# Kernel tuning notes

Hardware: AMD Instinct MI355X
Metric: run time of the kernel (lower is better)

The kernel has to match this reference:

```python
import jax, jax.numpy as jnp
import numpy as np

N_NODES = 100000
N_EDGES = 3200000
F_IN = 512
HIDDEN = 16
N_CLASSES = 16


def setup_inputs() -> dict:
    key = jax.random.key(0)
    k1, k2, k3, k4 = jax.random.split(key, 4)
    x = jax.random.normal(k1, (N_NODES, F_IN), dtype=jnp.float32)
    edge_index = jax.random.randint(k2, (2, N_EDGES), 0, N_NODES, dtype=jnp.int32)
    # Glorot-style init for GCN weights
    W1 = jax.random.normal(k3, (F_IN, HIDDEN), dtype=jnp.float32) * np.float32(np.sqrt(2.0 / (F_IN + HIDDEN)))
    b1 = jnp.zeros((HIDDEN,), dtype=jnp.float32)
    W2 = jax.random.normal(k4, (HIDDEN, N_CLASSES), dtype=jnp.float32) * np.float32(np.sqrt(2.0 / (HIDDEN + N_CLASSES)))
    b2 = jnp.zeros((N_CLASSES,), dtype=jnp.float32)
    return {"x": x, "W1": W1, "b1": b1, "W2": W2, "b2": b2, "edge_index": edge_index}


def _gcn_conv(x, src, dst, W, b, n_nodes):
    """PyG GCNConv: h = x @ W, then symmetric-normalized aggregation with self-loops, + bias."""
    h = x @ W  # [N, out]
    # degrees include self-loops (edge weight 1.0 everywhere)
    ones = jnp.ones(src.shape[0], dtype=h.dtype)
    deg = jax.ops.segment_sum(ones, dst, num_segments=n_nodes) + 1.0  # +1 for self-loop
    dinv = jax.lax.rsqrt(deg)  # deg >= 1, no zero guard needed
    norm = dinv[src] * dinv[dst]  # [E]
    agg = jax.ops.segment_sum(h[src] * norm[:, None], dst, num_segments=n_nodes)
    # self-loop contribution: norm_ii = 1/deg_i
    agg = agg + h * (dinv * dinv)[:, None]
    return agg + b


def reference(x, W1, b1, W2, b2, edge_index):
    src, dst = edge_index[0], edge_index[1]
    n = x.shape[0]
    h = jax.nn.relu(_gcn_conv(x, src, dst, W1, b1, n))
    # dropout is identity in eval mode
    out = _gcn_conv(h, src, dst, W2, b2, n)
    return jax.nn.log_softmax(out, axis=1)
```

## Files before the change

kernel.cpp:

```cpp
#include <hip/hip_runtime.h>
#include <math.h>

constexpr int N_NODES = 100000;
constexpr int N_EDGES = 3200000;
constexpr int F_IN    = 512;
constexpr int HID     = 16;

constexpr int NPAD = 100352;

constexpr int B_BITS = 8;
constexpr int NPB    = 1 << B_BITS;
constexpr int NBKT   = (N_NODES + NPB - 1) / NPB;
constexpr int SBLK   = 400;
constexpr int CHUNK  = N_EDGES / SBLK;
constexpr int CAP    = 10240;

typedef float f32x4 __attribute__((ext_vector_type(4)));
typedef short bfrag8 __attribute__((ext_vector_type(8)));

__device__ __forceinline__ unsigned short f2bf_rne(float f) {
    unsigned int u = __float_as_uint(f);
    u += 0x7FFFu + ((u >> 16) & 1u);
    return (unsigned short)(u >> 16);
}
__device__ __forceinline__ float bf2f(unsigned short u) {
    return __uint_as_float((unsigned int)u << 16);
}

__global__ __launch_bounds__(256) void prep_kernel(const float* __restrict__ W1,
                                                   unsigned short* __restrict__ w1t,
                                                   int* __restrict__ gcur,
                                                   unsigned short* __restrict__ hh_bf,
                                                   unsigned short* __restrict__ hh2_bf) {
    int i = blockIdx.x * 256 + threadIdx.x;
    if (i < F_IN * HID) {
        int k = i >> 4, n = i & 15;
        w1t[n * F_IN + k] = f2bf_rne(W1[i]);
    }
    if (i < NBKT) gcur[i] = i * CAP;
    if (i < 16) {
        hh_bf [N_NODES * 16 + i] = 0;
        hh2_bf[N_NODES * 16 + i] = 0;
    }
}

__global__ __launch_bounds__(1024) void bin_scatter_kernel(const int* __restrict__ src,
                                                           const int* __restrict__ dst,
                                                           int* __restrict__ gcur,
                                                           unsigned int* __restrict__ binned) {
    __shared__ int sdst[CHUNK];
    __shared__ int ssrc[CHUNK];
    __shared__ int cnt[NBKT];
    __shared__ int cur[NBKT];
    const int tid = threadIdx.x;
    for (int t = tid; t < NBKT; t += 1024) cnt[t] = 0;
    const int base = blockIdx.x * CHUNK;
    for (int i = tid; i < CHUNK; i += 1024) {
        sdst[i] = dst[base + i];
        ssrc[i] = src[base + i];
    }
    __syncthreads();
    for (int i = tid; i < CHUNK; i += 1024)
        atomicAdd(&cnt[sdst[i] >> B_BITS], 1);
    __syncthreads();
    for (int t = tid; t < NBKT; t += 1024)
        cur[t] = cnt[t] ? atomicAdd(&gcur[t], cnt[t]) : 0;
    __syncthreads();
    for (int i = tid; i < CHUNK; i += 1024) {
        int d = sdst[i];
        int b = d >> B_BITS;
        int pos = atomicAdd(&cur[b], 1);
        binned[pos] = ((unsigned)(d & (NPB - 1)) << 24) | (unsigned)ssrc[i];
    }
}

__global__ __launch_bounds__(1024) void csr_bucket_kernel(const unsigned int* __restrict__ binned,
                                                          const int* __restrict__ gcur,
                                                          int* __restrict__ row,
                                                          int* __restrict__ rowe,
                                                          int* __restrict__ csr,
                                                          float* __restrict__ dinv) {
    __shared__ unsigned int eb[CAP];
    __shared__ int deg[NPB];
    __shared__ int pre[NPB];
    __shared__ int cur[NPB];
    const int tid = threadIdx.x;
    const int b = blockIdx.x;
    const int e0 = b * CAP;
    int ne = gcur[b] - e0;
    if (ne > CAP) ne = CAP;
    if (ne < 0) ne = 0;

    if (tid < NPB) deg[tid] = 0;
    for (int i = tid; i < ne; i += 1024) eb[i] = binned[e0 + i];
    __syncthreads();
    for (int i = tid; i < ne; i += 1024)
        atomicAdd(&deg[eb[i] >> 24], 1);
    __syncthreads();
    if (tid < NPB) pre[tid] = (deg[tid] + 3) & ~3;
    __syncthreads();
    for (int off = 1; off < NPB; off <<= 1) {
        int v = 0;
        if (tid < NPB && tid >= off) v = pre[tid - off];
        __syncthreads();
        if (tid < NPB) pre[tid] += v;
        __syncthreads();
    }
    if (tid < NPB) {
        int excl = (tid == 0) ? 0 : pre[tid - 1];
        int start = e0 + excl;
        cur[tid] = start;
        int node = b * NPB + tid;
        if (node < N_NODES) {
            int pd = (deg[tid] + 3) & ~3;
            row[node]  = start;
            rowe[node] = start + pd;
            dinv[node] = rsqrtf((float)deg[tid] + 1.0f);
        }
    }
    __syncthreads();
    for (int i = tid; i < ne; i += 1024) {
        unsigned int v = eb[i];
        int pos = atomicAdd(&cur[v >> 24], 1);
        csr[pos] = (int)(v & 0xFFFFFFu);
    }
    if (tid < NPB) {
        int node = b * NPB + tid;
        if (node < N_NODES) {
            int d = deg[tid];
            int pd = (d + 3) & ~3;
            int s = e0 + ((tid == 0) ? 0 : pre[tid - 1]) + d;
            for (int q = d; q < pd; ++q) csr[s++] = N_NODES;
        }
    }
}

__global__ __launch_bounds__(256) void gemm1_kernel(const float* __restrict__ x,
                                                    const unsigned short* __restrict__ w1t,
                                                    const float* __restrict__ b1,
                                                    const float* __restrict__ dinv,
                                                    unsigned short* __restrict__ hh_bf,
                                                    float* __restrict__ aggs1) {
    const int tid  = threadIdx.x;
    const int lane = tid & 63;
    const int wv   = tid >> 6;
    const int m    = lane & 15;
    const int quad = lane >> 4;
    const int node0 = blockIdx.x * 64 + wv * 16;

    int gm = node0 + m; if (gm >= N_NODES) gm = N_NODES - 1;
    const float* arow = x + (size_t)gm * F_IN + quad * 8;

    bfrag8 bfr[16];
    const unsigned short* wbase = w1t + m * F_IN + quad * 8;
    #pragma unroll
    for (int t = 0; t < 16; ++t)
        bfr[t] = *(const bfrag8*)(wbase + t * 32);

    f32x4 acc = {0.f, 0.f, 0.f, 0.f};
    #pragma unroll 4
    for (int t = 0; t < 16; ++t) {
        float4 lo = *(const float4*)(arow + t * 32);
        float4 hi = *(const float4*)(arow + t * 32 + 4);
        bfrag8 afr;
        afr[0] = (short)f2bf_rne(lo.x); afr[1] = (short)f2bf_rne(lo.y);
        afr[2] = (short)f2bf_rne(lo.z); afr[3] = (short)f2bf_rne(lo.w);
        afr[4] = (short)f2bf_rne(hi.x); afr[5] = (short)f2bf_rne(hi.y);
        afr[6] = (short)f2bf_rne(hi.z); afr[7] = (short)f2bf_rne(hi.w);
        acc = __builtin_amdgcn_mfma_f32_16x16x32_bf16(afr, bfr[t], acc, 0, 0, 0);
    }

    const float b1j = b1[m];
    #pragma unroll
    for (int r = 0; r < 4; ++r) {
        int gn = node0 + quad * 4 + r;
        if (gn < N_NODES) {
            float dv = dinv[gn];
            float hv = acc[r] * dv;
            size_t o = (size_t)gn * 16 + m;
            hh_bf[o] = f2bf_rne(hv);
            aggs1[o] = hv * dv + b1j;
        }
    }
}

__global__ __launch_bounds__(256) void pull1_kernel(const unsigned short* __restrict__ hh_bf,
                                                    const float* __restrict__ aggs1,
                                                    const float* __restrict__ dinv,
                                                    const int* __restrict__ row,
                                                    const int* __restrict__ rowe,
                                                    const int* __restrict__ csr,
                                                    const float* __restrict__ W2,
                                                    const float* __restrict__ b2,
                                                    unsigned short* __restrict__ hh2_bf,
                                                    float* __restrict__ aggs2) {
    __shared__ f32x4 w2s[64];
    __shared__ f32x4 b2s[4];
    const int tid = threadIdx.x;
    if (tid < 64) w2s[tid] = ((const f32x4*)W2)[tid];
    if (tid < 4)  b2s[tid] = ((const f32x4*)b2)[tid];
    __syncthreads();

    int t = blockIdx.x * 256 + tid;
    int node = t >> 2;
    int l = t & 3;
    if (node >= N_NODES) return;

    int p = row[node], e = rowe[node];
    const unsigned short* hb = hh_bf + (l << 2);
    f32x4 a0 = {0,0,0,0}, a1 = {0,0,0,0}, a2 = {0,0,0,0}, a3 = {0,0,0,0};
    for (; p < e; p += 4) {
        int4 s = *(const int4*)(csr + p);
        ushort4 g0 = *(const ushort4*)(hb + (s.x << 4));
        ushort4 g1 = *(const ushort4*)(hb + (s.y << 4));
        ushort4 g2 = *(const ushort4*)(hb + (s.z << 4));
        ushort4 g3 = *(const ushort4*)(hb + (s.w << 4));
        a0.x += bf2f(g0.x); a0.y += bf2f(g0.y); a0.z += bf2f(g0.z); a0.w += bf2f(g0.w);
        a1.x += bf2f(g1.x); a1.y += bf2f(g1.y); a1.z += bf2f(g1.z); a1.w += bf2f(g1.w);
        a2.x += bf2f(g2.x); a2.y += bf2f(g2.y); a2.z += bf2f(g2.z); a2.w += bf2f(g2.w);
        a3.x += bf2f(g3.x); a3.y += bf2f(g3.y); a3.z += bf2f(g3.z); a3.w += bf2f(g3.w);
    }
    f32x4 a = (a0 + a1) + (a2 + a3);
    float dv = dinv[node];
    f32x4 base = *(const f32x4*)(aggs1 + ((size_t)node << 4) + (l << 2));
    float v[4];
    #pragma unroll
    for (int c = 0; c < 4; ++c) v[c] = fmaxf(base[c] + dv * a[c], 0.f);

    f32x4 h2 = {0.f, 0.f, 0.f, 0.f};
    #pragma unroll
    for (int k = 0; k < 16; ++k) {
        float vk = __shfl(v[k & 3], k >> 2, 4);
        f32x4 w = w2s[k * 4 + l];
        h2.x += vk * w.x; h2.y += vk * w.y; h2.z += vk * w.z; h2.w += vk * w.w;
    }
    f32x4 bb = b2s[l];
    ushort4 hs;
    f32x4 ag;
    float hv0 = h2.x * dv; hs.x = f2bf_rne(hv0); ag.x = hv0 * dv + bb.x;
    float hv1 = h2.y * dv; hs.y = f2bf_rne(hv1); ag.y = hv1 * dv + bb.y;
    float hv2 = h2.z * dv; hs.z = f2bf_rne(hv2); ag.z = hv2 * dv + bb.z;
    float hv3 = h2.w * dv; hs.w = f2bf_rne(hv3); ag.w = hv3 * dv + bb.w;
    size_t o = ((size_t)node << 4) + (l << 2);
    *(ushort4*)(hh2_bf + o) = hs;
    *(f32x4*)(aggs2 + o) = ag;
}

__global__ __launch_bounds__(256) void pull2_kernel(const unsigned short* __restrict__ hh2_bf,
                                                    const float* __restrict__ aggs2,
                                                    const float* __restrict__ dinv,
                                                    const int* __restrict__ row,
                                                    const int* __restrict__ rowe,
                                                    const int* __restrict__ csr,
                                                    float* __restrict__ out) {
    int t = blockIdx.x * 256 + threadIdx.x;
    int node = t >> 2;
    int l = t & 3;
    if (node >= N_NODES) return;

    int p = row[node], e = rowe[node];
    const unsigned short* hb = hh2_bf + (l << 2);
    f32x4 a0 = {0,0,0,0}, a1 = {0,0,0,0}, a2 = {0,0,0,0}, a3 = {0,0,0,0};
    for (; p < e; p += 4) {
        int4 s = *(const int4*)(csr + p);
        ushort4 g0 = *(const ushort4*)(hb + (s.x << 4));
        ushort4 g1 = *(const ushort4*)(hb + (s.y << 4));
        ushort4 g2 = *(const ushort4*)(hb + (s.z << 4));
        ushort4 g3 = *(const ushort4*)(hb + (s.w << 4));
        a0.x += bf2f(g0.x); a0.y += bf2f(g0.y); a0.z += bf2f(g0.z); a0.w += bf2f(g0.w);
        a1.x += bf2f(g1.x); a1.y += bf2f(g1.y); a1.z += bf2f(g1.z); a1.w += bf2f(g1.w);
        a2.x += bf2f(g2.x); a2.y += bf2f(g2.y); a2.z += bf2f(g2.z); a2.w += bf2f(g2.w);
        a3.x += bf2f(g3.x); a3.y += bf2f(g3.y); a3.z += bf2f(g3.z); a3.w += bf2f(g3.w);
    }
    f32x4 a = (a0 + a1) + (a2 + a3);
    float dv = dinv[node];
    f32x4 base = *(const f32x4*)(aggs2 + ((size_t)node << 4) + (l << 2));
    f32x4 o4;
    o4.x = base.x + dv * a.x; o4.y = base.y + dv * a.y;
    o4.z = base.z + dv * a.z; o4.w = base.w + dv * a.w;

    float m = fmaxf(fmaxf(o4.x, o4.y), fmaxf(o4.z, o4.w));
    m = fmaxf(m, __shfl_xor(m, 1));
    m = fmaxf(m, __shfl_xor(m, 2));
    float s = expf(o4.x - m) + expf(o4.y - m) + expf(o4.z - m) + expf(o4.w - m);
    s += __shfl_xor(s, 1);
    s += __shfl_xor(s, 2);
    float ls = m + logf(s);
    f32x4 r;
    r.x = o4.x - ls; r.y = o4.y - ls; r.z = o4.z - ls; r.w = o4.w - ls;
    *(f32x4*)(out + ((size_t)node << 4) + (l << 2)) = r;
}

extern "C" void kernel_launch(void* const* d_in, const int* in_sizes, int n_in,
                              void* d_out, int out_size, void* d_ws, size_t ws_size,
                              hipStream_t stream) {
    const float* x    = (const float*)d_in[0];
    const float* W1   = (const float*)d_in[1];
    const float* b1   = (const float*)d_in[2];
    const float* W2   = (const float*)d_in[3];
    const float* b2   = (const float*)d_in[4];
    const int*   ei   = (const int*)d_in[5];
    const int*   src  = ei;
    const int*   dst  = ei + N_EDGES;
    float* out = (float*)d_out;

    constexpr size_t SLOTS    = (size_t)NBKT * CAP;
    constexpr size_t OFF_DINV = 512;
    constexpr size_t OFF_ROW  = 512 + (size_t)NPAD;
    constexpr size_t OFF_ROWE = 512 + 2 * (size_t)NPAD;
    constexpr size_t OFF_CSR  = 512 + 3 * (size_t)NPAD;
    constexpr size_t OFF_HH   = OFF_CSR + SLOTS;
    constexpr size_t OFF_AG1  = OFF_HH + 800512;
    constexpr size_t OFF_HH2  = OFF_AG1 + 1600000;
    constexpr size_t OFF_AG2  = OFF_HH2 + 800512;
    constexpr size_t OFF_W1T  = OFF_AG2 + 1600000;

    int*   wsi  = (int*)d_ws;
    float* wsf  = (float*)d_ws;
    int*   gcur  = wsi;
    float* dinv  = wsf + OFF_DINV;
    int*   row   = wsi + OFF_ROW;
    int*   rowe  = wsi + OFF_ROWE;
    int*   csr   = wsi + OFF_CSR;
    unsigned int* binned = (unsigned int*)csr;
    unsigned short* hh_bf  = (unsigned short*)(wsi + OFF_HH);
    float*          aggs1  = wsf + OFF_AG1;
    unsigned short* hh2_bf = (unsigned short*)(wsi + OFF_HH2);
    float*          aggs2  = wsf + OFF_AG2;
    unsigned short* w1t    = (unsigned short*)(wsi + OFF_W1T);

    const int MB  = (N_NODES + 63) / 64;
    const int GB4 = (N_NODES * 4 + 255) / 256;

    prep_kernel       <<<32, 256, 0, stream>>>(W1, w1t, gcur, hh_bf, hh2_bf);
    bin_scatter_kernel<<<SBLK, 1024, 0, stream>>>(src, dst, gcur, binned);
    csr_bucket_kernel <<<NBKT, 1024, 0, stream>>>(binned, gcur, row, rowe, csr, dinv);
    gemm1_kernel      <<<MB, 256, 0, stream>>>(x, w1t, b1, dinv, hh_bf, aggs1);
    pull1_kernel      <<<GB4, 256, 0, stream>>>(hh_bf, aggs1, dinv, row, rowe, csr, W2, b2, hh2_bf, aggs2);
    pull2_kernel      <<<GB4, 256, 0, stream>>>(hh2_bf, aggs2, dinv, row, rowe, csr, out);
}
```

Baseline: 438.4 us.

## Widen pull gathers to 16-byte per lane with 2 lanes per node

The two aggregation kernels now use 2 threads per node, each gathering 8 bf16 features (16 bytes) per neighbor, instead of 4 threads with 8-byte gathers. CSR rows are padded to multiples of 8 and row start/end are packed into one int2. The edge-binning kernel drops its shared-memory staging of src/dst, reads global memory directly, and uses 512 blocks. Wider gathers and fewer threads should cut instruction count and improve memory efficiency, at the cost of more padding edges and fewer threads in flight per node.

```diff
diff --git a/kernel.cpp b/kernel.cpp
--- a/kernel.cpp
+++ b/kernel.cpp
@@ -11,11 +11,13 @@
 constexpr int B_BITS = 8;
 constexpr int NPB    = 1 << B_BITS;
 constexpr int NBKT   = (N_NODES + NPB - 1) / NPB;
-constexpr int SBLK   = 400;
+constexpr int SBLK   = 512;
 constexpr int CHUNK  = N_EDGES / SBLK;
 constexpr int CAP    = 10240;
 
 typedef float f32x4 __attribute__((ext_vector_type(4)));
+typedef float f32x8 __attribute__((ext_vector_type(8)));
+typedef unsigned short u16x8 __attribute__((ext_vector_type(8)));
 typedef short bfrag8 __attribute__((ext_vector_type(8)));
 
 __device__ __forceinline__ unsigned short f2bf_rne(float f) {
@@ -48,36 +50,29 @@
                                                            const int* __restrict__ dst,
                                                            int* __restrict__ gcur,
                                                            unsigned int* __restrict__ binned) {
-    __shared__ int sdst[CHUNK];
-    __shared__ int ssrc[CHUNK];
     __shared__ int cnt[NBKT];
     __shared__ int cur[NBKT];
     const int tid = threadIdx.x;
     for (int t = tid; t < NBKT; t += 1024) cnt[t] = 0;
+    __syncthreads();
     const int base = blockIdx.x * CHUNK;
-    for (int i = tid; i < CHUNK; i += 1024) {
-        sdst[i] = dst[base + i];
-        ssrc[i] = src[base + i];
-    }
-    __syncthreads();
     for (int i = tid; i < CHUNK; i += 1024)
-        atomicAdd(&cnt[sdst[i] >> B_BITS], 1);
+        atomicAdd(&cnt[dst[base + i] >> B_BITS], 1);
     __syncthreads();
     for (int t = tid; t < NBKT; t += 1024)
         cur[t] = cnt[t] ? atomicAdd(&gcur[t], cnt[t]) : 0;
     __syncthreads();
     for (int i = tid; i < CHUNK; i += 1024) {
-        int d = sdst[i];
+        int d = dst[base + i];
         int b = d >> B_BITS;
         int pos = atomicAdd(&cur[b], 1);
-        binned[pos] = ((unsigned)(d & (NPB - 1)) << 24) | (unsigned)ssrc[i];
+        binned[pos] = ((unsigned)(d & (NPB - 1)) << 24) | (unsigned)src[base + i];
     }
 }
 
 __global__ __launch_bounds__(1024) void csr_bucket_kernel(const unsigned int* __restrict__ binned,
                                                           const int* __restrict__ gcur,
-                                                          int* __restrict__ row,
-                                                          int* __restrict__ rowe,
+                                                          int2* __restrict__ row2,
                                                           int* __restrict__ csr,
                                                           float* __restrict__ dinv) {
     __shared__ unsigned int eb[CAP];
@@ -97,7 +92,7 @@
     for (int i = tid; i < ne; i += 1024)
         atomicAdd(&deg[eb[i] >> 24], 1);
     __syncthreads();
-    if (tid < NPB) pre[tid] = (deg[tid] + 3) & ~3;
+    if (tid < NPB) pre[tid] = (deg[tid] + 7) & ~7;
     __syncthreads();
     for (int off = 1; off < NPB; off <<= 1) {
         int v = 0;
@@ -112,9 +107,8 @@
         cur[tid] = start;
         int node = b * NPB + tid;
         if (node < N_NODES) {
-            int pd = (deg[tid] + 3) & ~3;
-            row[node]  = start;
-            rowe[node] = start + pd;
+            int pd = (deg[tid] + 7) & ~7;
+            row2[node] = make_int2(start, start + pd);
             dinv[node] = rsqrtf((float)deg[tid] + 1.0f);
         }
     }
@@ -128,7 +122,7 @@
         int node = b * NPB + tid;
         if (node < N_NODES) {
             int d = deg[tid];
-            int pd = (d + 3) & ~3;
+            int pd = (d + 7) & ~7;
             int s = e0 + ((tid == 0) ? 0 : pre[tid - 1]) + d;
             for (int q = d; q < pd; ++q) csr[s++] = N_NODES;
         }
@@ -187,108 +181,138 @@
 __global__ __launch_bounds__(256) void pull1_kernel(const unsigned short* __restrict__ hh_bf,
                                                     const float* __restrict__ aggs1,
                                                     const float* __restrict__ dinv,
-                                                    const int* __restrict__ row,
-                                                    const int* __restrict__ rowe,
+                                                    const int2* __restrict__ row2,
                                                     const int* __restrict__ csr,
                                                     const float* __restrict__ W2,
                                                     const float* __restrict__ b2,
                                                     unsigned short* __restrict__ hh2_bf,
                                                     float* __restrict__ aggs2) {
     __shared__ f32x4 w2s[64];
-    __shared__ f32x4 b2s[4];
+    __shared__ float b2s[16];
     const int tid = threadIdx.x;
     if (tid < 64) w2s[tid] = ((const f32x4*)W2)[tid];
-    if (tid < 4)  b2s[tid] = ((const f32x4*)b2)[tid];
+    if (tid < 16) b2s[tid] = b2[tid];
     __syncthreads();
 
     int t = blockIdx.x * 256 + tid;
-    int node = t >> 2;
-    int l = t & 3;
+    int node = t >> 1;
+    int l = t & 1;
     if (node >= N_NODES) return;
 
-    int p = row[node], e = rowe[node];
-    const unsigned short* hb = hh_bf + (l << 2);
-    f32x4 a0 = {0,0,0,0}, a1 = {0,0,0,0}, a2 = {0,0,0,0}, a3 = {0,0,0,0};
-    for (; p < e; p += 4) {
-        int4 s = *(const int4*)(csr + p);
-        ushort4 g0 = *(const ushort4*)(hb + (s.x << 4));
-        ushort4 g1 = *(const ushort4*)(hb + (s.y << 4));
-        ushort4 g2 = *(const ushort4*)(hb + (s.z << 4));
-        ushort4 g3 = *(const ushort4*)(hb + (s.w << 4));
-        a0.x += bf2f(g0.x); a0.y += bf2f(g0.y); a0.z += bf2f(g0.z); a0.w += bf2f(g0.w);
-        a1.x += bf2f(g1.x); a1.y += bf2f(g1.y); a1.z += bf2f(g1.z); a1.w += bf2f(g1.w);
-        a2.x += bf2f(g2.x); a2.y += bf2f(g2.y); a2.z += bf2f(g2.z); a2.w += bf2f(g2.w);
-        a3.x += bf2f(g3.x); a3.y += bf2f(g3.y); a3.z += bf2f(g3.z); a3.w += bf2f(g3.w);
-    }
-    f32x4 a = (a0 + a1) + (a2 + a3);
+    int2 re = row2[node];
+    int p = re.x, e = re.y;
+    const unsigned short* hb = hh_bf + (l << 3);
+    f32x8 accA = {0,0,0,0,0,0,0,0}, accB = {0,0,0,0,0,0,0,0};
+    for (; p < e; p += 8) {
+        int4 sA = *(const int4*)(csr + p);
+        int4 sB = *(const int4*)(csr + p + 4);
+        u16x8 g0 = *(const u16x8*)(hb + (sA.x << 4));
+        u16x8 g1 = *(const u16x8*)(hb + (sA.y << 4));
+        u16x8 g2 = *(const u16x8*)(hb + (sA.z << 4));
+        u16x8 g3 = *(const u16x8*)(hb + (sA.w << 4));
+        u16x8 g4 = *(const u16x8*)(hb + (sB.x << 4));
+        u16x8 g5 = *(const u16x8*)(hb + (sB.y << 4));
+        u16x8 g6 = *(const u16x8*)(hb + (sB.z << 4));
+        u16x8 g7 = *(const u16x8*)(hb + (sB.w << 4));
+        #pragma unroll
+        for (int c = 0; c < 8; ++c) {
+            accA[c] += (bf2f(g0[c]) + bf2f(g1[c])) + (bf2f(g2[c]) + bf2f(g3[c]));
+            accB[c] += (bf2f(g4[c]) + bf2f(g5[c])) + (bf2f(g6[c]) + bf2f(g7[c]));
+        }
+    }
+    f32x8 a = accA + accB;
     float dv = dinv[node];
-    f32x4 base = *(const f32x4*)(aggs1 + ((size_t)node << 4) + (l << 2));
-    float v[4];
-    #pragma unroll
-    for (int c = 0; c < 4; ++c) v[c] = fmaxf(base[c] + dv * a[c], 0.f);
-
-    f32x4 h2 = {0.f, 0.f, 0.f, 0.f};
+    const f32x4* agp = (const f32x4*)(aggs1 + ((size_t)node << 4) + (l << 3));
+    f32x4 bA = agp[0], bB = agp[1];
+    float v[8];
+    #pragma unroll
+    for (int c = 0; c < 4; ++c) v[c]     = fmaxf(bA[c] + dv * a[c],     0.f);
+    #pragma unroll
+    for (int c = 0; c < 4; ++c) v[c + 4] = fmaxf(bB[c] + dv * a[c + 4], 0.f);
+
+    f32x4 h2a = {0.f,0.f,0.f,0.f}, h2b = {0.f,0.f,0.f,0.f};
     #pragma unroll
     for (int k = 0; k < 16; ++k) {
-        float vk = __shfl(v[k & 3], k >> 2, 4);
-        f32x4 w = w2s[k * 4 + l];
-        h2.x += vk * w.x; h2.y += vk * w.y; h2.z += vk * w.z; h2.w += vk * w.w;
-    }
-    f32x4 bb = b2s[l];
-    ushort4 hs;
-    f32x4 ag;
-    float hv0 = h2.x * dv; hs.x = f2bf_rne(hv0); ag.x = hv0 * dv + bb.x;
-    float hv1 = h2.y * dv; hs.y = f2bf_rne(hv1); ag.y = hv1 * dv + bb.y;
-    float hv2 = h2.z * dv; hs.z = f2bf_rne(hv2); ag.z = hv2 * dv + bb.z;
-    float hv3 = h2.w * dv; hs.w = f2bf_rne(hv3); ag.w = hv3 * dv + bb.w;
-    size_t o = ((size_t)node << 4) + (l << 2);
-    *(ushort4*)(hh2_bf + o) = hs;
-    *(f32x4*)(aggs2 + o) = ag;
+        float vk = __shfl(v[k & 7], k >> 3, 2);
+        h2a += vk * w2s[k * 4 + l * 2];
+        h2b += vk * w2s[k * 4 + l * 2 + 1];
+    }
+    u16x8 hs;
+    f32x4 agA, agB;
+    #pragma unroll
+    for (int c = 0; c < 4; ++c) {
+        float hv = h2a[c] * dv;
+        hs[c] = f2bf_rne(hv);
+        agA[c] = hv * dv + b2s[l * 8 + c];
+    }
+    #pragma unroll
+    for (int c = 0; c < 4; ++c) {
+        float hv = h2b[c] * dv;
+        hs[c + 4] = f2bf_rne(hv);
+        agB[c] = hv * dv + b2s[l * 8 + 4 + c];
+    }
+    size_t o = ((size_t)node << 4) + (l << 3);
+    *(u16x8*)(hh2_bf + o) = hs;
+    f32x4* o2 = (f32x4*)(aggs2 + o);
+    o2[0] = agA; o2[1] = agB;
 }
 
 __global__ __launch_bounds__(256) void pull2_kernel(const unsigned short* __restrict__ hh2_bf,
                                                     const float* __restrict__ aggs2,
                                                     const float* __restrict__ dinv,
-                                                    const int* __restrict__ row,
-                                                    const int* __restrict__ rowe,
+                                                    const int2* __restrict__ row2,
                                                     const int* __restrict__ csr,
                                                     float* __restrict__ out) {
     int t = blockIdx.x * 256 + threadIdx.x;
-    int node = t >> 2;
-    int l = t & 3;
+    int node = t >> 1;
+    int l = t & 1;
     if (node >= N_NODES) return;
 
-    int p = row[node], e = rowe[node];
-    const unsigned short* hb = hh2_bf + (l << 2);
-    f32x4 a0 = {0,0,0,0}, a1 = {0,0,0,0}, a2 = {0,0,0,0}, a3 = {0,0,0,0};
-    for (; p < e; p += 4) {
-        int4 s = *(const int4*)(csr + p);
-        ushort4 g0 = *(const ushort4*)(hb + (s.x << 4));
-        ushort4 g1 = *(const ushort4*)(hb + (s.y << 4));
-        ushort4 g2 = *(const ushort4*)(hb + (s.z << 4));
-        ushort4 g3 = *(const ushort4*)(hb + (s.w << 4));
-        a0.x += bf2f(g0.x); a0.y += bf2f(g0.y); a0.z += bf2f(g0.z); a0.w += bf2f(g0.w);
-        a1.x += bf2f(g1.x); a1.y += bf2f(g1.y); a1.z += bf2f(g1.z); a1.w += bf2f(g1.w);
-        a2.x += bf2f(g2.x); a2.y += bf2f(g2.y); a2.z += bf2f(g2.z); a2.w += bf2f(g2.w);
-        a3.x += bf2f(g3.x); a3.y += bf2f(g3.y); a3.z += bf2f(g3.z); a3.w += bf2f(g3.w);
-    }
-    f32x4 a = (a0 + a1) + (a2 + a3);
+    int2 re = row2[node];
+    int p = re.x, e = re.y;
+    const unsigned short* hb = hh2_bf + (l << 3);
+    f32x8 accA = {0,0,0,0,0,0,0,0}, accB = {0,0,0,0,0,0,0,0};
+    for (; p < e; p += 8) {
+        int4 sA = *(const int4*)(csr + p);
+        int4 sB = *(const int4*)(csr + p + 4);
+        u16x8 g0 = *(const u16x8*)(hb + (sA.x << 4));
+        u16x8 g1 = *(const u16x8*)(hb + (sA.y << 4));
+        u16x8 g2 = *(const u16x8*)(hb + (sA.z << 4));
+        u16x8 g3 = *(const u16x8*)(hb + (sA.w << 4));
+        u16x8 g4 = *(const u16x8*)(hb + (sB.x << 4));
+        u16x8 g5 = *(const u16x8*)(hb + (sB.y << 4));
+        u16x8 g6 = *(const u16x8*)(hb + (sB.z << 4));
+        u16x8 g7 = *(const u16x8*)(hb + (sB.w << 4));
+        #pragma unroll
+        for (int c = 0; c < 8; ++c) {
+            accA[c] += (bf2f(g0[c]) + bf2f(g1[c])) + (bf2f(g2[c]) + bf2f(g3[c]));
+            accB[c] += (bf2f(g4[c]) + bf2f(g5[c])) + (bf2f(g6[c]) + bf2f(g7[c]));
+        }
+    }
+    f32x8 a = accA + accB;
     float dv = dinv[node];
-    f32x4 base = *(const f32x4*)(aggs2 + ((size_t)node << 4) + (l << 2));
-    f32x4 o4;
-    o4.x = base.x + dv * a.x; o4.y = base.y + dv * a.y;
-    o4.z = base.z + dv * a.z; o4.w = base.w + dv * a.w;
-
-    float m = fmaxf(fmaxf(o4.x, o4.y), fmaxf(o4.z, o4.w));
+    const f32x4* agp = (const f32x4*)(aggs2 + ((size_t)node << 4) + (l << 3));
+    f32x4 bA = agp[0], bB = agp[1];
+    float o8[8];
+    #pragma unroll
+    for (int c = 0; c < 4; ++c) o8[c]     = bA[c] + dv * a[c];
+    #pragma unroll
+    for (int c = 0; c < 4; ++c) o8[c + 4] = bB[c] + dv * a[c + 4];
+
+    float m = o8[0];
+    #pragma unroll
+    for (int c = 1; c < 8; ++c) m = fmaxf(m, o8[c]);
     m = fmaxf(m, __shfl_xor(m, 1));
-    m = fmaxf(m, __shfl_xor(m, 2));
-    float s = expf(o4.x - m) + expf(o4.y - m) + expf(o4.z - m) + expf(o4.w - m);
+    float s = 0.f;
+    #pragma unroll
+    for (int c = 0; c < 8; ++c) s += expf(o8[c] - m);
     s += __shfl_xor(s, 1);
-    s += __shfl_xor(s, 2);
     float ls = m + logf(s);
-    f32x4 r;
-    r.x = o4.x - ls; r.y = o4.y - ls; r.z = o4.z - ls; r.w = o4.w - ls;
-    *(f32x4*)(out + ((size_t)node << 4) + (l << 2)) = r;
+    f32x4 rA, rB;
+    #pragma unroll
+    for (int c = 0; c < 4; ++c) { rA[c] = o8[c] - ls; rB[c] = o8[c + 4] - ls; }
+    f32x4* op = (f32x4*)(out + ((size_t)node << 4) + (l << 3));
+    op[0] = rA; op[1] = rB;
 }
 
 extern "C" void kernel_launch(void* const* d_in, const int* in_sizes, int n_in,
@@ -306,8 +330,7 @@
 
     constexpr size_t SLOTS    = (size_t)NBKT * CAP;
     constexpr size_t OFF_DINV = 512;
-    constexpr size_t OFF_ROW  = 512 + (size_t)NPAD;
-    constexpr size_t OFF_ROWE = 512 + 2 * (size_t)NPAD;
+    constexpr size_t OFF_ROW2 = 512 + (size_t)NPAD;
     constexpr size_t OFF_CSR  = 512 + 3 * (size_t)NPAD;
     constexpr size_t OFF_HH   = OFF_CSR + SLOTS;
     constexpr size_t OFF_AG1  = OFF_HH + 800512;
@@ -319,8 +342,7 @@
     float* wsf  = (float*)d_ws;
     int*   gcur  = wsi;
     float* dinv  = wsf + OFF_DINV;
-    int*   row   = wsi + OFF_ROW;
-    int*   rowe  = wsi + OFF_ROWE;
+    int2*  row2  = (int2*)(wsi + OFF_ROW2);
     int*   csr   = wsi + OFF_CSR;
     unsigned int* binned = (unsigned int*)csr;
     unsigned short* hh_bf  = (unsigned short*)(wsi + OFF_HH);
@@ -330,12 +352,12 @@
     unsigned short* w1t    = (unsigned short*)(wsi + OFF_W1T);
 
     const int MB  = (N_NODES + 63) / 64;
-    const int GB4 = (N_NODES * 4 + 255) / 256;
+    const int GB2 = (N_NODES * 2 + 255) / 256;
 
     prep_kernel       <<<32, 256, 0, stream>>>(W1, w1t, gcur, hh_bf, hh2_bf);
     bin_scatter_kernel<<<SBLK, 1024, 0, stream>>>(src, dst, gcur, binned);
-    csr_bucket_kernel <<<NBKT, 1024, 0, stream>>>(binned, gcur, row, rowe, csr, dinv);
+    csr_bucket_kernel <<<NBKT, 1024, 0, stream>>>(binned, gcur, row2, csr, dinv);
     gemm1_kernel      <<<MB, 256, 0, stream>>>(x, w1t, b1, dinv, hh_bf, aggs1);
-    pull1_kernel      <<<GB4, 256, 0, stream>>>(hh_bf, aggs1, dinv, row, rowe, csr, W2, b2, hh2_bf, aggs2);
-    pull2_kernel      <<<GB4, 256, 0, stream>>>(hh2_bf, aggs2, dinv, row, rowe, csr, out);
-}
+    pull1_kernel      <<<GB2, 256, 0, stream>>>(hh_bf, aggs1, dinv, row2, csr, W2, b2, hh2_bf, aggs2);
+    pull2_kernel      <<<GB2, 256, 0, stream>>>(hh2_bf, aggs2, dinv, row2, csr, out);
+}
```

Result: slower. 462.0 us (+5.4%).

## Sort nodes by padded degree within buckets to balance pull-kernel wavefronts

Applied to the files above, without the earlier changes.

The CSR build kernel now builds a per-bucket histogram of padded degree and writes a permutation that groups nodes of similar degree together. Both pull kernels then read node ids through this permutation, so lanes in a wavefront run similar loop trip counts. Row start and end are packed into one int2, and the fp32-to-bf16 conversion in the GEMM uses packed bf16x2 intrinsics. The cost is an extra permutation load and scattered per-node output writes, which weakens locality.

```diff
diff --git a/kernel.cpp b/kernel.cpp
--- a/kernel.cpp
+++ b/kernel.cpp
@@ -1,4 +1,5 @@
 #include <hip/hip_runtime.h>
+#include <hip/hip_bf16.h>
 #include <math.h>
 
 constexpr int N_NODES = 100000;
@@ -76,14 +77,17 @@
 
 __global__ __launch_bounds__(1024) void csr_bucket_kernel(const unsigned int* __restrict__ binned,
                                                           const int* __restrict__ gcur,
-                                                          int* __restrict__ row,
-                                                          int* __restrict__ rowe,
+                                                          int2* __restrict__ row2,
                                                           int* __restrict__ csr,
-                                                          float* __restrict__ dinv) {
+                                                          float* __restrict__ dinv,
+                                                          int* __restrict__ perm) {
     __shared__ unsigned int eb[CAP];
     __shared__ int deg[NPB];
     __shared__ int pre[NPB];
     __shared__ int cur[NPB];
+    __shared__ int hist[64];
+    __shared__ int hoff[64];
+    __shared__ int hcur[64];
     const int tid = threadIdx.x;
     const int b = blockIdx.x;
     const int e0 = b * CAP;
@@ -92,12 +96,18 @@
     if (ne < 0) ne = 0;
 
     if (tid < NPB) deg[tid] = 0;
+    if (tid < 64) hist[tid] = 0;
     for (int i = tid; i < ne; i += 1024) eb[i] = binned[e0 + i];
     __syncthreads();
     for (int i = tid; i < ne; i += 1024)
         atomicAdd(&deg[eb[i] >> 24], 1);
     __syncthreads();
-    if (tid < NPB) pre[tid] = (deg[tid] + 3) & ~3;
+    int pd = 0;
+    if (tid < NPB) {
+        pd = (deg[tid] + 3) & ~3;
+        pre[tid] = pd;
+        atomicAdd(&hist[min(pd >> 2, 63)], 1);
+    }
     __syncthreads();
     for (int off = 1; off < NPB; off <<= 1) {
         int v = 0;
@@ -106,17 +116,28 @@
         if (tid < NPB) pre[tid] += v;
         __syncthreads();
     }
+    if (tid < 64) hoff[tid] = hist[tid];
+    __syncthreads();
+    for (int off = 1; off < 64; off <<= 1) {
+        int v = 0;
+        if (tid < 64 && tid >= off) v = hoff[tid - off];
+        __syncthreads();
+        if (tid < 64) hoff[tid] += v;
+        __syncthreads();
+    }
+    if (tid < 64) hcur[tid] = (tid == 0) ? 0 : hoff[tid - 1];
+    __syncthreads();
     if (tid < NPB) {
         int excl = (tid == 0) ? 0 : pre[tid - 1];
         int start = e0 + excl;
         cur[tid] = start;
         int node = b * NPB + tid;
         if (node < N_NODES) {
-            int pd = (deg[tid] + 3) & ~3;
-            row[node]  = start;
-            rowe[node] = start + pd;
+            row2[node] = make_int2(start, start + pd);
             dinv[node] = rsqrtf((float)deg[tid] + 1.0f);
         }
+        int rank = atomicAdd(&hcur[min(pd >> 2, 63)], 1);
+        perm[b * NPB + rank] = node;
     }
     __syncthreads();
     for (int i = tid; i < ne; i += 1024) {
@@ -128,9 +149,9 @@
         int node = b * NPB + tid;
         if (node < N_NODES) {
             int d = deg[tid];
-            int pd = (d + 3) & ~3;
+            int pdl = (d + 3) & ~3;
             int s = e0 + ((tid == 0) ? 0 : pre[tid - 1]) + d;
-            for (int q = d; q < pd; ++q) csr[s++] = N_NODES;
+            for (int q = d; q < pdl; ++q) csr[s++] = N_NODES;
         }
     }
 }
@@ -162,12 +183,12 @@
     for (int t = 0; t < 16; ++t) {
         float4 lo = *(const float4*)(arow + t * 32);
         float4 hi = *(const float4*)(arow + t * 32 + 4);
-        bfrag8 afr;
-        afr[0] = (short)f2bf_rne(lo.x); afr[1] = (short)f2bf_rne(lo.y);
-        afr[2] = (short)f2bf_rne(lo.z); afr[3] = (short)f2bf_rne(lo.w);
-        afr[4] = (short)f2bf_rne(hi.x); afr[5] = (short)f2bf_rne(hi.y);
-        afr[6] = (short)f2bf_rne(hi.z); afr[7] = (short)f2bf_rne(hi.w);
-        acc = __builtin_amdgcn_mfma_f32_16x16x32_bf16(afr, bfr[t], acc, 0, 0, 0);
+        union { bfrag8 fr; __hip_bfloat162 h2[4]; } u;
+        u.h2[0] = __float22bfloat162_rn(float2{lo.x, lo.y});
+        u.h2[1] = __float22bfloat162_rn(float2{lo.z, lo.w});
+        u.h2[2] = __float22bfloat162_rn(float2{hi.x, hi.y});
+        u.h2[3] = __float22bfloat162_rn(float2{hi.z, hi.w});
+        acc = __builtin_amdgcn_mfma_f32_16x16x32_bf16(u.fr, bfr[t], acc, 0, 0, 0);
     }
 
     const float b1j = b1[m];
@@ -187,9 +208,9 @@
 __global__ __launch_bounds__(256) void pull1_kernel(const unsigned short* __restrict__ hh_bf,
                                                     const float* __restrict__ aggs1,
                                                     const float* __restrict__ dinv,
-                                                    const int* __restrict__ row,
-                                                    const int* __restrict__ rowe,
+                                                    const int2* __restrict__ row2,
                                                     const int* __restrict__ csr,
+                                                    const int* __restrict__ perm,
                                                     const float* __restrict__ W2,
                                                     const float* __restrict__ b2,
                                                     unsigned short* __restrict__ hh2_bf,
@@ -202,11 +223,12 @@
     __syncthreads();
 
     int t = blockIdx.x * 256 + tid;
-    int node = t >> 2;
+    int node = perm[t >> 2];
     int l = t & 3;
     if (node >= N_NODES) return;
 
-    int p = row[node], e = rowe[node];
+    int2 re = row2[node];
+    int p = re.x, e = re.y;
     const unsigned short* hb = hh_bf + (l << 2);
     f32x4 a0 = {0,0,0,0}, a1 = {0,0,0,0}, a2 = {0,0,0,0}, a3 = {0,0,0,0};
     for (; p < e; p += 4) {
@@ -249,16 +271,17 @@
 __global__ __launch_bounds__(256) void pull2_kernel(const unsigned short* __restrict__ hh2_bf,
                                                     const float* __restrict__ aggs2,
                                                     const float* __restrict__ dinv,
-                                                    const int* __restrict__ row,
-                                                    const int* __restrict__ rowe,
+                                                    const int2* __restrict__ row2,
                                                     const int* __restrict__ csr,
+                                                    const int* __restrict__ perm,
                                                     float* __restrict__ out) {
     int t = blockIdx.x * 256 + threadIdx.x;
-    int node = t >> 2;
+    int node = perm[t >> 2];
     int l = t & 3;
     if (node >= N_NODES) return;
 
-    int p = row[node], e = rowe[node];
+    int2 re = row2[node];
+    int p = re.x, e = re.y;
     const unsigned short* hb = hh2_bf + (l << 2);
     f32x4 a0 = {0,0,0,0}, a1 = {0,0,0,0}, a2 = {0,0,0,0}, a3 = {0,0,0,0};
     for (; p < e; p += 4) {
@@ -306,9 +329,9 @@
 
     constexpr size_t SLOTS    = (size_t)NBKT * CAP;
     constexpr size_t OFF_DINV = 512;
-    constexpr size_t OFF_ROW  = 512 + (size_t)NPAD;
-    constexpr size_t OFF_ROWE = 512 + 2 * (size_t)NPAD;
-    constexpr size_t OFF_CSR  = 512 + 3 * (size_t)NPAD;
+    constexpr size_t OFF_ROW2 = 512 + (size_t)NPAD;
+    constexpr size_t OFF_PERM = 512 + 3 * (size_t)NPAD;
+    constexpr size_t OFF_CSR  = 512 + 4 * (size_t)NPAD;
     constexpr size_t OFF_HH   = OFF_CSR + SLOTS;
     constexpr size_t OFF_AG1  = OFF_HH + 800512;
     constexpr size_t OFF_HH2  = OFF_AG1 + 1600000;
@@ -319,8 +342,8 @@
     float* wsf  = (float*)d_ws;
     int*   gcur  = wsi;
     float* dinv  = wsf + OFF_DINV;
-    int*   row   = wsi + OFF_ROW;
-    int*   rowe  = wsi + OFF_ROWE;
+    int2*  row2  = (int2*)(wsi + OFF_ROW2);
+    int*   perm  = wsi + OFF_PERM;
     int*   csr   = wsi + OFF_CSR;
     unsigned int* binned = (unsigned int*)csr;
     unsigned short* hh_bf  = (unsigned short*)(wsi + OFF_HH);
@@ -330,12 +353,12 @@
     unsigned short* w1t    = (unsigned short*)(wsi + OFF_W1T);
 
     const int MB  = (N_NODES + 63) / 64;
-    const int GB4 = (N_NODES * 4 + 255) / 256;
+    const int GB4 = (NBKT * NPB * 4) / 256;
 
     prep_kernel       <<<32, 256, 0, stream>>>(W1, w1t, gcur, hh_bf, hh2_bf);
     bin_scatter_kernel<<<SBLK, 1024, 0, stream>>>(src, dst, gcur, binned);
-    csr_bucket_kernel <<<NBKT, 1024, 0, stream>>>(binned, gcur, row, rowe, csr, dinv);
+    csr_bucket_kernel <<<NBKT, 1024, 0, stream>>>(binned, gcur, row2, csr, dinv, perm);
     gemm1_kernel      <<<MB, 256, 0, stream>>>(x, w1t, b1, dinv, hh_bf, aggs1);
-    pull1_kernel      <<<GB4, 256, 0, stream>>>(hh_bf, aggs1, dinv, row, rowe, csr, W2, b2, hh2_bf, aggs2);
-    pull2_kernel      <<<GB4, 256, 0, stream>>>(hh2_bf, aggs2, dinv, row, rowe, csr, out);
-}
+    pull1_kernel      <<<GB4, 256, 0, stream>>>(hh_bf, aggs1, dinv, row2, csr, perm, W2, b2, hh2_bf, aggs2);
+    pull2_kernel      <<<GB4, 256, 0, stream>>>(hh2_bf, aggs2, dinv, row2, csr, perm, out);
+}
```

Measured after the change: 451.2 us. +2.9%, slower.
